# Kernel tuning notes

Hardware: AMD Instinct MI355X
Metric: run time of the kernel (lower is better)

The kernel has to match this reference:

```python
import jax, jax.numpy as jnp
import numpy as np

E = 2048      # embed_dim
HQ = 32       # num_query_heads
HKV = 8       # num_kv_heads
DH = E // HQ  # head_dim = 64
G = HQ // HKV # group_size = 4
KV_DIM = E * HKV // HQ  # 512
B, S = 2, 2048


def setup_inputs() -> dict:
    key = jax.random.key(0)
    ks = jax.random.split(key, 11)
    sc_in = 1.0 / np.sqrt(E)
    sc_attn = 1.0 / np.sqrt(E)
    return {
        "query": jax.random.normal(ks[0], (B, S, E), jnp.float32),
        "key": jax.random.normal(ks[1], (B, S, E), jnp.float32),
        "value": jax.random.normal(ks[2], (B, S, E), jnp.float32),
        "Wq": jax.random.normal(ks[3], (E, E), jnp.float32) * sc_in,
        "bq": jnp.zeros((E,), jnp.float32),
        "Wk": jax.random.normal(ks[4], (E, KV_DIM), jnp.float32) * sc_in,
        "bk": jnp.zeros((KV_DIM,), jnp.float32),
        "Wv": jax.random.normal(ks[5], (E, KV_DIM), jnp.float32) * sc_in,
        "bv": jnp.zeros((KV_DIM,), jnp.float32),
        "Wo": jax.random.normal(ks[6], (E, E), jnp.float32) * sc_attn,
        "bo": jnp.zeros((E,), jnp.float32),
    }


def reference(query, key, value, Wq, bq, Wk, bk, Wv, bv, Wo, bo):
    b, s, _ = query.shape
    # projections
    Q = (query @ Wq + bq).reshape(b, s, HQ, DH).transpose(0, 2, 1, 3)   # [B,HQ,S,DH]
    K = (key @ Wk + bk).reshape(b, s, HKV, DH).transpose(0, 2, 1, 3)    # [B,HKV,S,DH]
    V = (value @ Wv + bv).reshape(b, s, HKV, DH).transpose(0, 2, 1, 3)  # [B,HKV,S,DH]
    # GQA: repeat_interleave along head dim (kv head h -> query heads h*G..h*G+G-1)
    K = jnp.repeat(K, G, axis=1)  # [B,HQ,S,DH]
    V = jnp.repeat(V, G, axis=1)  # [B,HQ,S,DH]
    scores = jnp.einsum('bhqd,bhkd->bhqk', Q, K) / np.sqrt(DH).astype(np.float32)
    attn_weights = jax.nn.softmax(scores, axis=-1)                      # [B,HQ,S,S]
    attn_out = jnp.einsum('bhqk,bhkd->bhqd', attn_weights, V)           # [B,HQ,S,DH]
    attn_out = attn_out.transpose(0, 2, 1, 3).reshape(b, s, E)
    out = attn_out @ Wo + bo
    return out, attn_weights
```

## Files before the change

kernel.cpp:

```cpp
#include <hip/hip_runtime.h>
#include <stdint.h>

typedef _Float16 f16;
typedef _Float16 f16x8 __attribute__((ext_vector_type(8)));
typedef _Float16 f16x4 __attribute__((ext_vector_type(4)));
typedef float    f32x4 __attribute__((ext_vector_type(4)));

#define SEQ   2048
#define EDIM  2048
#define NHQ   32
#define NHKV  8
#define DHEAD 64
#define KVD   512
#define NB    2
#define NTOK  (NB*SEQ)
#define SCALE 0.1803368801111204f

__device__ __forceinline__ f32x4 mfma16(f16x8 a, f16x8 b, f32x4 c) {
  return __builtin_amdgcn_mfma_f32_16x16x32_f16(a, b, c, 0, 0, 0);
}

__device__ __forceinline__ void gload_lds16(const void* g, void* l) {
  __builtin_amdgcn_global_load_lds(
      (const __attribute__((address_space(1))) void*)g,
      (__attribute__((address_space(3))) void*)l, 16, 0, 0);
}

__global__ __launch_bounds__(256) void k_cvt3(const float* __restrict__ s0,
                                              const float* __restrict__ s1,
                                              const float* __restrict__ s2,
                                              f16* __restrict__ d) {
  int i = blockIdx.x * 256 + threadIdx.x;
  int t = i >> 21, j = i & ((1 << 21) - 1);
  const float* s = (t == 0) ? s0 : ((t == 1) ? s1 : s2);
  float4 v = reinterpret_cast<const float4*>(s)[j];
  f16x4 h;
  h[0] = (f16)v.x; h[1] = (f16)v.y; h[2] = (f16)v.z; h[3] = (f16)v.w;
  reinterpret_cast<f16x4*>(d)[i] = h;
}

__global__ __launch_bounds__(256) void k_tconv(const float* __restrict__ s0,
                                               const float* __restrict__ s1,
                                               f16* __restrict__ d0,
                                               f16* __restrict__ d1,
                                               int R, int C) {
  const float* s = blockIdx.z ? s1 : s0;
  f16* d = blockIdx.z ? d1 : d0;
  __shared__ float t[32][33];
  int tr = blockIdx.x, tc = blockIdx.y;
  int lr = threadIdx.x >> 3;
  int lc = (threadIdx.x & 7) << 2;
  float4 v = *reinterpret_cast<const float4*>(&s[(size_t)(tr*32+lr)*C + tc*32 + lc]);
  t[lr][lc+0] = v.x; t[lr][lc+1] = v.y; t[lr][lc+2] = v.z; t[lr][lc+3] = v.w;
  __syncthreads();
  f16x4 h;
  h[0] = (f16)t[lc+0][lr];
  h[1] = (f16)t[lc+1][lr];
  h[2] = (f16)t[lc+2][lr];
  h[3] = (f16)t[lc+3][lr];
  *reinterpret_cast<f16x4*>(&d[(size_t)(tc*32+lr)*R + tr*32 + lc]) = h;
}

__global__ __launch_bounds__(256) void k_trv(const f16* __restrict__ src,
                                             f16* __restrict__ dst) {
  __shared__ f16 t[64][68];
  int bh = blockIdx.x;
  int st = blockIdx.y;
  int b = bh >> 3, h = bh & 7;
  #pragma unroll
  for (int i = 0; i < 4; ++i) {
    int sl = i*16 + (threadIdx.x >> 4);
    int d4 = (threadIdx.x & 15) * 4;
    *(f16x4*)&t[sl][d4] =
        *(const f16x4*)&src[(size_t)(b*SEQ + st*64 + sl)*KVD + h*DHEAD + d4];
  }
  __syncthreads();
  #pragma unroll
  for (int i = 0; i < 4; ++i) {
    int dl = i*16 + (threadIdx.x >> 4);
    int s4 = (threadIdx.x & 15) * 4;
    f16x4 v;
    v[0] = t[s4+0][dl]; v[1] = t[s4+1][dl]; v[2] = t[s4+2][dl]; v[3] = t[s4+3][dl];
    *(f16x4*)&dst[(size_t)(bh*DHEAD + dl)*SEQ + st*64 + s4] = v;
  }
}

template<int F16OUT>
__global__ __launch_bounds__(256) void k_gemm(
    const f16* __restrict__ A0, const f16* __restrict__ A1,
    const f16* __restrict__ Bt0, const f16* __restrict__ Bt1,
    const float* __restrict__ bias0, const float* __restrict__ bias1,
    void* __restrict__ C0, void* __restrict__ C1,
    int M, int N, int K)
{
  const f16* A    = blockIdx.z ? A1 : A0;
  const f16* Bt   = blockIdx.z ? Bt1 : Bt0;
  const float* bias = blockIdx.z ? bias1 : bias0;
  void* Cout      = blockIdx.z ? C1 : C0;

  __shared__ f16 sA[128*64];
  __shared__ f16 sB[128*64];
  const int tid  = threadIdx.x;
  const int lane = tid & 63, wv = tid >> 6;
  const int tn = blockIdx.x, tm = blockIdx.y;
  const int wm = wv >> 1, wn = wv & 1;
  const int l15 = lane & 15, lhi = lane >> 4;

  const f32x4 zz = {0.f, 0.f, 0.f, 0.f};
  f32x4 acc[4][4];
  #pragma unroll
  for (int m = 0; m < 4; ++m)
    #pragma unroll
    for (int n = 0; n < 4; ++n) acc[m][n] = zz;

  const f16* gsrc[8];
  f16* ldst[8];
  #pragma unroll
  for (int i = 0; i < 8; ++i) {
    int u = wv*8 + i;
    int r  = (u & 15)*8 + (lane >> 3);
    int cb = ((lane & 7) << 4) ^ ((r & 7) << 4);
    if (u < 16) {
      gsrc[i] = A  + (size_t)(tm*128 + r)*K + (cb >> 1);
      ldst[i] = sA + u*512;
    } else {
      gsrc[i] = Bt + (size_t)(tn*128 + r)*K + (cb >> 1);
      ldst[i] = sB + (u - 16)*512;
    }
  }

  int aoff[2][4], boff[2][4];
  #pragma unroll
  for (int ks = 0; ks < 2; ++ks)
    #pragma unroll
    for (int m = 0; m < 4; ++m) {
      int ra = wm*64 + m*16 + l15;
      aoff[ks][m] = ra*128 + ((ks*64 + (lhi << 4)) ^ ((ra & 7) << 4));
      int rb = wn*64 + m*16 + l15;
      boff[ks][m] = rb*128 + ((ks*64 + (lhi << 4)) ^ ((rb & 7) << 4));
    }

  const int nkb = K >> 6;
  for (int kb = 0; kb < nkb; ++kb) {
    #pragma unroll
    for (int i = 0; i < 8; ++i)
      gload_lds16(gsrc[i] + kb*64, ldst[i]);
    __syncthreads();
    #pragma unroll
    for (int ks = 0; ks < 2; ++ks) {
      f16x8 af[4], bf[4];
      #pragma unroll
      for (int m = 0; m < 4; ++m)
        af[m] = *(const f16x8*)((const char*)sA + aoff[ks][m]);
      #pragma unroll
      for (int n = 0; n < 4; ++n)
        bf[n] = *(const f16x8*)((const char*)sB + boff[ks][n]);
      #pragma unroll
      for (int m = 0; m < 4; ++m)
        #pragma unroll
        for (int n = 0; n < 4; ++n)
          acc[m][n] = mfma16(af[m], bf[n], acc[m][n]);
    }
    __syncthreads();
  }

  float bcol[4];
  #pragma unroll
  for (int n = 0; n < 4; ++n)
    bcol[n] = bias[tn*128 + wn*64 + n*16 + l15];
  #pragma unroll
  for (int m = 0; m < 4; ++m)
    #pragma unroll
    for (int n = 0; n < 4; ++n)
      #pragma unroll
      for (int r = 0; r < 4; ++r) {
        int row = tm*128 + wm*64 + m*16 + lhi*4 + r;
        int col = tn*128 + wn*64 + n*16 + l15;
        float v = acc[m][n][r] + bcol[n];
        if (F16OUT) ((f16*)Cout)[(size_t)row*N + col] = (f16)v;
        else        ((float*)Cout)[(size_t)row*N + col] = v;
      }
}

__global__ __launch_bounds__(256) void k_attn(
    const f16* __restrict__ Qp,
    const f16* __restrict__ Kp,
    const f16* __restrict__ Vt,
    float* __restrict__ wout,
    f16* __restrict__ AO)
{
  __shared__ f16 sK[2][64*64];
  __shared__ f16 sV[2][64*64];
  __shared__ f16 sW[4][16*64];
  const int tid = threadIdx.x, lane = tid & 63, wv = tid >> 6;
  const int bid = (blockIdx.x & 7) * 256 + (blockIdx.x >> 3);
  const int b = bid >> 10, h = (bid >> 5) & 31, qb = bid & 31;
  const int hk = h >> 2;
  const int l15 = lane & 15, lhi = lane >> 4;
  const int rloc = (lane >> 3) & 7, chk = lane & 7;
  const int csw = (chk ^ rloc) * 8;
  const int sw  = (l15 & 7) << 4;
  const int qrow0 = qb*64 + wv*16;
  const f32x4 zz = {0.f, 0.f, 0.f, 0.f};

  f16x8 qf[2];
  #pragma unroll
  for (int ks = 0; ks < 2; ++ks)
    qf[ks] = *(const f16x8*)&Qp[(size_t)(b*SEQ + qrow0 + l15)*EDIM
                                + h*DHEAD + ks*32 + lhi*8];

  const f16* Kb = Kp + (size_t)(b*SEQ)*KVD + hk*DHEAD;
  const f16* Vb = Vt + (size_t)((b*NHKV + hk)*DHEAD)*SEQ;

  float lsum = 0.f;
  {
    #pragma unroll
    for (int i = 0; i < 2; ++i) {
      int u = wv*2 + i;
      gload_lds16(Kb + (size_t)(u*8 + rloc)*KVD + csw, &sK[0][u*512]);
    }
    __syncthreads();
    int buf = 0;
    for (int kb = 0; kb < SEQ/64; ++kb) {
      if (kb < SEQ/64 - 1) {
        #pragma unroll
        for (int i = 0; i < 2; ++i) {
          int u = wv*2 + i;
          gload_lds16(Kb + (size_t)((kb+1)*64 + u*8 + rloc)*KVD + csw, &sK[buf^1][u*512]);
        }
      }
      #pragma unroll
      for (int kt = 0; kt < 4; ++kt) {
        const char* kbase = (const char*)&sK[buf][0] + (kt*16 + l15)*128;
        f16x8 kf0 = *(const f16x8*)(kbase + ((lhi*16) ^ sw));
        f16x8 kf1 = *(const f16x8*)(kbase + ((64 + lhi*16) ^ sw));
        f32x4 s = zz;
        s = mfma16(kf0, qf[0], s);
        s = mfma16(kf1, qf[1], s);
        #pragma unroll
        for (int r = 0; r < 4; ++r)
          lsum += __builtin_amdgcn_exp2f(s[r] * SCALE);
      }
      __syncthreads();
      buf ^= 1;
    }
  }
  float den = lsum;
  den += __shfl_xor(den, 16);
  den += __shfl_xor(den, 32);
  const float rinv = __builtin_amdgcn_rcpf(den);

  f32x4 o[4];
  #pragma unroll
  for (int dt = 0; dt < 4; ++dt) o[dt] = zz;

  f16* swv = &sW[wv][0];
  float* wrow = wout + (size_t)((b*NHQ + h)*SEQ + qrow0)*SEQ;

  {
    #pragma unroll
    for (int i = 0; i < 2; ++i) {
      int u = wv*2 + i;
      gload_lds16(Kb + (size_t)(u*8 + rloc)*KVD + csw, &sK[0][u*512]);
      gload_lds16(Vb + (size_t)(u*8 + rloc)*SEQ + csw, &sV[0][u*512]);
    }
    __syncthreads();
    int buf = 0;
    for (int kb = 0; kb < SEQ/64; ++kb) {
      if (kb < SEQ/64 - 1) {
        #pragma unroll
        for (int i = 0; i < 2; ++i) {
          int u = wv*2 + i;
          gload_lds16(Kb + (size_t)((kb+1)*64 + u*8 + rloc)*KVD + csw, &sK[buf^1][u*512]);
          gload_lds16(Vb + (size_t)(u*8 + rloc)*SEQ + (kb+1)*64 + csw, &sV[buf^1][u*512]);
        }
      }
      #pragma unroll
      for (int kt = 0; kt < 4; ++kt) {
        const char* kbase = (const char*)&sK[buf][0] + (kt*16 + l15)*128;
        f16x8 kf0 = *(const f16x8*)(kbase + ((lhi*16) ^ sw));
        f16x8 kf1 = *(const f16x8*)(kbase + ((64 + lhi*16) ^ sw));
        f32x4 s = zz;
        s = mfma16(kf0, qf[0], s);
        s = mfma16(kf1, qf[1], s);
        f32x4 wvec;
        f16x4 wh;
        #pragma unroll
        for (int r = 0; r < 4; ++r) {
          float w = __builtin_amdgcn_exp2f(s[r] * SCALE) * rinv;
          wvec[r] = w;
          wh[r] = (f16)w;
        }
        __builtin_nontemporal_store(wvec,
            (f32x4*)(wrow + (size_t)l15*SEQ + kb*64 + kt*16 + lhi*4));
        *(f16x4*)((char*)swv + l15*128 + ((kt*32 + lhi*8) ^ sw)) = wh;
      }
      #pragma unroll
      for (int ks = 0; ks < 2; ++ks) {
        f16x8 af = *(const f16x8*)((const char*)swv + l15*128 + ((ks*64 + lhi*16) ^ sw));
        #pragma unroll
        for (int dt = 0; dt < 4; ++dt) {
          const char* vbase = (const char*)&sV[buf][0] + (dt*16 + l15)*128;
          f16x8 vf = *(const f16x8*)(vbase + ((ks*64 + lhi*16) ^ sw));
          o[dt] = mfma16(af, vf, o[dt]);
        }
      }
      __syncthreads();
      buf ^= 1;
    }
  }

  #pragma unroll
  for (int dt = 0; dt < 4; ++dt)
    #pragma unroll
    for (int r = 0; r < 4; ++r)
      AO[(size_t)(b*SEQ + qrow0 + lhi*4 + r)*EDIM + h*DHEAD + dt*16 + l15]
          = (f16)o[dt][r];
}

extern "C" void kernel_launch(void* const* d_in, const int* in_sizes, int n_in,
                              void* d_out, int out_size, void* d_ws, size_t ws_size,
                              hipStream_t stream) {
  (void)in_sizes; (void)n_in; (void)out_size; (void)ws_size;
  const float* query = (const float*)d_in[0];
  const float* key   = (const float*)d_in[1];
  const float* value = (const float*)d_in[2];
  const float* Wq    = (const float*)d_in[3];
  const float* bq    = (const float*)d_in[4];
  const float* Wk    = (const float*)d_in[5];
  const float* bk    = (const float*)d_in[6];
  const float* Wv    = (const float*)d_in[7];
  const float* bv    = (const float*)d_in[8];
  const float* Wo    = (const float*)d_in[9];
  const float* bo    = (const float*)d_in[10];

  float* out   = (float*)d_out;
  float* wattn = out + (size_t)NTOK*EDIM;

  f16* p   = (f16*)d_ws;
  f16* q16 = p;  p += (size_t)NTOK*EDIM;
  f16* k16 = p;  p += (size_t)NTOK*EDIM;
  f16* v16 = p;  p += (size_t)NTOK*EDIM;
  f16* wqT = p;  p += (size_t)EDIM*EDIM;
  f16* wkT = p;  p += (size_t)KVD*EDIM;
  f16* wvT = p;  p += (size_t)KVD*EDIM;
  f16* woT = p;  p += (size_t)EDIM*EDIM;
  f16* Qp  = p;  p += (size_t)NTOK*EDIM;
  f16* Kp  = p;  p += (size_t)NTOK*KVD;
  f16* Vp  = p;  p += (size_t)NTOK*KVD;
  f16* Vt  = p;  p += (size_t)NTOK*KVD;
  f16* AO  = p;  p += (size_t)NTOK*EDIM;

  k_cvt3<<<3*(NTOK*EDIM/4)/256, 256, 0, stream>>>(query, key, value, q16);

  k_tconv<<<dim3(EDIM/32, EDIM/32, 2), 256, 0, stream>>>(Wq, Wo, wqT, woT, EDIM, EDIM);
  k_tconv<<<dim3(EDIM/32, KVD/32, 2),  256, 0, stream>>>(Wk, Wv, wkT, wvT, EDIM, KVD);

  k_gemm<1><<<dim3(EDIM/128, NTOK/128, 1), 256, 0, stream>>>(
      q16, q16, wqT, wqT, bq, bq, Qp, Qp, NTOK, EDIM, EDIM);
  k_gemm<1><<<dim3(KVD/128, NTOK/128, 2), 256, 0, stream>>>(
      k16, v16, wkT, wvT, bk, bv, Kp, Vp, NTOK, KVD, EDIM);

  k_trv<<<dim3(NB*NHKV, SEQ/64), 256, 0, stream>>>(Vp, Vt);

  k_attn<<<NB*NHQ*(SEQ/64), 256, 0, stream>>>(Qp, Kp, Vt, wattn, AO);

  k_gemm<0><<<dim3(EDIM/128, NTOK/128, 1), 256, 0, stream>>>(
      AO, AO, woT, woT, bo, bo, out, out, NTOK, EDIM, EDIM);
}
```

Baseline: 508.5 us.

## Fuse QKV projections into one 256-tile pipelined GEMM and deepen attention prefetch

Replaces the 128x128 GEMM with a 256-row, 512-thread GEMM that runs a 4-stage LDS pipeline with explicit vmcnt waits. Q, K and V projections now run as a single launch writing one packed QKV buffer, relying on wqT/wkT/wvT being contiguous so they form a 3072-column B matrix. The attention kernel reads from the packed layout and replaces its trailing __syncthreads with a partial vmcnt wait plus barrier so prefetches can stay in flight. The aim is more operand reuse per tile, fewer launches and more load/compute overlap. The cost is higher register and LDS pressure, and the manual waitcnt counts and the workspace layout both have to be exactly right.

```diff
diff --git a/kernel.cpp b/kernel.cpp
--- a/kernel.cpp
+++ b/kernel.cpp
@@ -14,6 +14,7 @@
 #define KVD   512
 #define NB    2
 #define NTOK  (NB*SEQ)
+#define QKVN  3072
 #define SCALE 0.1803368801111204f
 
 __device__ __forceinline__ f32x4 mfma16(f16x8 a, f16x8 b, f32x4 c) {
@@ -61,7 +62,7 @@
   *reinterpret_cast<f16x4*>(&d[(size_t)(tc*32+lr)*R + tr*32 + lc]) = h;
 }
 
-__global__ __launch_bounds__(256) void k_trv(const f16* __restrict__ src,
+__global__ __launch_bounds__(256) void k_trv(const f16* __restrict__ qkv,
                                              f16* __restrict__ dst) {
   __shared__ f16 t[64][68];
   int bh = blockIdx.x;
@@ -72,7 +73,7 @@
     int sl = i*16 + (threadIdx.x >> 4);
     int d4 = (threadIdx.x & 15) * 4;
     *(f16x4*)&t[sl][d4] =
-        *(const f16x4*)&src[(size_t)(b*SEQ + st*64 + sl)*KVD + h*DHEAD + d4];
+        *(const f16x4*)&qkv[(size_t)(b*SEQ + st*64 + sl)*QKVN + 2560 + h*DHEAD + d4];
   }
   __syncthreads();
   #pragma unroll
@@ -85,106 +86,132 @@
   }
 }
 
-template<int F16OUT>
-__global__ __launch_bounds__(256) void k_gemm(
-    const f16* __restrict__ A0, const f16* __restrict__ A1,
-    const f16* __restrict__ Bt0, const f16* __restrict__ Bt1,
-    const float* __restrict__ bias0, const float* __restrict__ bias1,
-    void* __restrict__ C0, void* __restrict__ C1,
-    int M, int N, int K)
+template<int BN, int F16OUT, int NTN>
+__global__ __launch_bounds__(512, 2) void k_gemm256(
+    const f16* __restrict__ Abase, const f16* __restrict__ Bt,
+    const float* __restrict__ bq, const float* __restrict__ bk,
+    const float* __restrict__ bv, void* __restrict__ Cout)
 {
-  const f16* A    = blockIdx.z ? A1 : A0;
-  const f16* Bt   = blockIdx.z ? Bt1 : Bt0;
-  const float* bias = blockIdx.z ? bias1 : bias0;
-  void* Cout      = blockIdx.z ? C1 : C0;
-
-  __shared__ f16 sA[128*64];
-  __shared__ f16 sB[128*64];
-  const int tid  = threadIdx.x;
-  const int lane = tid & 63, wv = tid >> 6;
-  const int tn = blockIdx.x, tm = blockIdx.y;
-  const int wm = wv >> 1, wn = wv & 1;
+  constexpr int K   = EDIM;
+  constexpr int NT  = K / 32;
+  constexpr int NLB = BN / 128;
+  constexpr int NI  = BN / 64;
+  constexpr int NCOL = NTN * BN;
+
+  __shared__ f16 sA[4][256*32];
+  __shared__ f16 sB[4][BN*32];
+
+  const int tid = threadIdx.x, lane = tid & 63, w = tid >> 6;
+  const int cpx = gridDim.x >> 3;
+  const int flat = blockIdx.x;
+  const int tid2 = (flat & 7) * cpx + (flat >> 3);
+  const int tn = tid2 % NTN, tm = tid2 / NTN;
+
+  int sel = 0, coff = 0;
+  if (BN == 256) { sel = (tn >= 8) + (tn >= 10); coff = sel == 0 ? 0 : (sel == 1 ? 2048 : 2560); }
+  const f16* A = Abase + (size_t)sel * NTOK * EDIM;
+  const float* bias = sel == 0 ? bq : (sel == 1 ? bk : bv);
+
+  const int wm = w >> 2, wn = w & 3;
   const int l15 = lane & 15, lhi = lane >> 4;
 
+  const f16* gA[2]; int uA[2];
+  #pragma unroll
+  for (int r = 0; r < 2; ++r) {
+    int row = r*128 + w*16 + (lane >> 2);
+    gA[r] = A + (size_t)(tm*256 + row)*K + (((lane & 3) ^ (row & 3)) << 3);
+    uA[r] = row * 32;
+  }
+  const f16* gB[NLB]; int uB[NLB];
+  #pragma unroll
+  for (int r = 0; r < NLB; ++r) {
+    int row = r*128 + w*16 + (lane >> 2);
+    gB[r] = Bt + (size_t)(tn*BN + row)*K + (((lane & 3) ^ (row & 3)) << 3);
+    uB[r] = row * 32;
+  }
+
+  int aoff[8], boff[NI];
+  #pragma unroll
+  for (int mi = 0; mi < 8; ++mi)
+    aoff[mi] = (wm*128 + mi*16 + l15)*64 + ((lhi ^ (l15 & 3)) << 4);
+  #pragma unroll
+  for (int ni = 0; ni < NI; ++ni)
+    boff[ni] = (wn*(BN/4) + ni*16 + l15)*64 + ((lhi ^ (l15 & 3)) << 4);
+
   const f32x4 zz = {0.f, 0.f, 0.f, 0.f};
-  f32x4 acc[4][4];
-  #pragma unroll
-  for (int m = 0; m < 4; ++m)
-    #pragma unroll
-    for (int n = 0; n < 4; ++n) acc[m][n] = zz;
-
-  const f16* gsrc[8];
-  f16* ldst[8];
-  #pragma unroll
-  for (int i = 0; i < 8; ++i) {
-    int u = wv*8 + i;
-    int r  = (u & 15)*8 + (lane >> 3);
-    int cb = ((lane & 7) << 4) ^ ((r & 7) << 4);
-    if (u < 16) {
-      gsrc[i] = A  + (size_t)(tm*128 + r)*K + (cb >> 1);
-      ldst[i] = sA + u*512;
-    } else {
-      gsrc[i] = Bt + (size_t)(tn*128 + r)*K + (cb >> 1);
-      ldst[i] = sB + (u - 16)*512;
-    }
-  }
-
-  int aoff[2][4], boff[2][4];
-  #pragma unroll
-  for (int ks = 0; ks < 2; ++ks)
-    #pragma unroll
-    for (int m = 0; m < 4; ++m) {
-      int ra = wm*64 + m*16 + l15;
-      aoff[ks][m] = ra*128 + ((ks*64 + (lhi << 4)) ^ ((ra & 7) << 4));
-      int rb = wn*64 + m*16 + l15;
-      boff[ks][m] = rb*128 + ((ks*64 + (lhi << 4)) ^ ((rb & 7) << 4));
-    }
-
-  const int nkb = K >> 6;
-  for (int kb = 0; kb < nkb; ++kb) {
-    #pragma unroll
-    for (int i = 0; i < 8; ++i)
-      gload_lds16(gsrc[i] + kb*64, ldst[i]);
-    __syncthreads();
-    #pragma unroll
-    for (int ks = 0; ks < 2; ++ks) {
-      f16x8 af[4], bf[4];
-      #pragma unroll
-      for (int m = 0; m < 4; ++m)
-        af[m] = *(const f16x8*)((const char*)sA + aoff[ks][m]);
-      #pragma unroll
-      for (int n = 0; n < 4; ++n)
-        bf[n] = *(const f16x8*)((const char*)sB + boff[ks][n]);
-      #pragma unroll
-      for (int m = 0; m < 4; ++m)
-        #pragma unroll
-        for (int n = 0; n < 4; ++n)
-          acc[m][n] = mfma16(af[m], bf[n], acc[m][n]);
-    }
-    __syncthreads();
-  }
-
-  float bcol[4];
-  #pragma unroll
-  for (int n = 0; n < 4; ++n)
-    bcol[n] = bias[tn*128 + wn*64 + n*16 + l15];
-  #pragma unroll
-  for (int m = 0; m < 4; ++m)
-    #pragma unroll
-    for (int n = 0; n < 4; ++n)
+  f32x4 acc[8][NI];
+  #pragma unroll
+  for (int mi = 0; mi < 8; ++mi)
+    #pragma unroll
+    for (int ni = 0; ni < NI; ++ni) acc[mi][ni] = zz;
+
+  auto STAGE = [&](int t) {
+    int sl = t & 3;
+    #pragma unroll
+    for (int r = 0; r < 2; ++r)   gload_lds16(gA[r] + t*32, &sA[sl][uA[r]]);
+    #pragma unroll
+    for (int r = 0; r < NLB; ++r) gload_lds16(gB[r] + t*32, &sB[sl][uB[r]]);
+  };
+  auto COMP = [&](int t) {
+    int sl = t & 3;
+    const char* ba = (const char*)&sA[sl][0];
+    const char* bb = (const char*)&sB[sl][0];
+    f16x8 af[8], bf[NI];
+    #pragma unroll
+    for (int ni = 0; ni < NI; ++ni) bf[ni] = *(const f16x8*)(bb + boff[ni]);
+    #pragma unroll
+    for (int mi = 0; mi < 8; ++mi)  af[mi] = *(const f16x8*)(ba + aoff[mi]);
+    #pragma unroll
+    for (int mi = 0; mi < 8; ++mi)
+      #pragma unroll
+      for (int ni = 0; ni < NI; ++ni)
+        acc[mi][ni] = mfma16(af[mi], bf[ni], acc[mi][ni]);
+  };
+
+  STAGE(0); STAGE(1); STAGE(2);
+  for (int t = 0; t < NT - 3; ++t) {
+    if (BN == 256) asm volatile("s_waitcnt vmcnt(8)" ::: "memory");
+    else           asm volatile("s_waitcnt vmcnt(6)" ::: "memory");
+    __builtin_amdgcn_s_barrier();
+    __builtin_amdgcn_sched_barrier(0);
+    STAGE(t + 3);
+    COMP(t);
+  }
+  if (BN == 256) asm volatile("s_waitcnt vmcnt(8)" ::: "memory");
+  else           asm volatile("s_waitcnt vmcnt(6)" ::: "memory");
+  __builtin_amdgcn_s_barrier();
+  __builtin_amdgcn_sched_barrier(0);
+  COMP(NT - 3);
+  if (BN == 256) asm volatile("s_waitcnt vmcnt(4)" ::: "memory");
+  else           asm volatile("s_waitcnt vmcnt(3)" ::: "memory");
+  __builtin_amdgcn_s_barrier();
+  __builtin_amdgcn_sched_barrier(0);
+  COMP(NT - 2);
+  asm volatile("s_waitcnt vmcnt(0)" ::: "memory");
+  __builtin_amdgcn_s_barrier();
+  __builtin_amdgcn_sched_barrier(0);
+  COMP(NT - 1);
+
+  float bcol[NI];
+  #pragma unroll
+  for (int ni = 0; ni < NI; ++ni)
+    bcol[ni] = bias[tn*BN + wn*(BN/4) + ni*16 + l15 - coff];
+  #pragma unroll
+  for (int mi = 0; mi < 8; ++mi)
+    #pragma unroll
+    for (int ni = 0; ni < NI; ++ni)
       #pragma unroll
       for (int r = 0; r < 4; ++r) {
-        int row = tm*128 + wm*64 + m*16 + lhi*4 + r;
-        int col = tn*128 + wn*64 + n*16 + l15;
-        float v = acc[m][n][r] + bcol[n];
-        if (F16OUT) ((f16*)Cout)[(size_t)row*N + col] = (f16)v;
-        else        ((float*)Cout)[(size_t)row*N + col] = v;
+        int row = tm*256 + wm*128 + mi*16 + lhi*4 + r;
+        int col = tn*BN + wn*(BN/4) + ni*16 + l15;
+        float v = acc[mi][ni][r] + bcol[ni];
+        if (F16OUT) ((f16*)Cout)[(size_t)row*NCOL + col] = (f16)v;
+        else        ((float*)Cout)[(size_t)row*NCOL + col] = v;
       }
 }
 
 __global__ __launch_bounds__(256) void k_attn(
-    const f16* __restrict__ Qp,
-    const f16* __restrict__ Kp,
+    const f16* __restrict__ QKV,
     const f16* __restrict__ Vt,
     float* __restrict__ wout,
     f16* __restrict__ AO)
@@ -206,10 +233,10 @@
   f16x8 qf[2];
   #pragma unroll
   for (int ks = 0; ks < 2; ++ks)
-    qf[ks] = *(const f16x8*)&Qp[(size_t)(b*SEQ + qrow0 + l15)*EDIM
-                                + h*DHEAD + ks*32 + lhi*8];
-
-  const f16* Kb = Kp + (size_t)(b*SEQ)*KVD + hk*DHEAD;
+    qf[ks] = *(const f16x8*)&QKV[(size_t)(b*SEQ + qrow0 + l15)*QKVN
+                                 + h*DHEAD + ks*32 + lhi*8];
+
+  const f16* Kb = QKV + 2048 + (size_t)(b*SEQ)*QKVN + hk*DHEAD;
   const f16* Vb = Vt + (size_t)((b*NHKV + hk)*DHEAD)*SEQ;
 
   float lsum = 0.f;
@@ -217,7 +244,7 @@
     #pragma unroll
     for (int i = 0; i < 2; ++i) {
       int u = wv*2 + i;
-      gload_lds16(Kb + (size_t)(u*8 + rloc)*KVD + csw, &sK[0][u*512]);
+      gload_lds16(Kb + (size_t)(u*8 + rloc)*QKVN + csw, &sK[0][u*512]);
     }
     __syncthreads();
     int buf = 0;
@@ -226,7 +253,7 @@
         #pragma unroll
         for (int i = 0; i < 2; ++i) {
           int u = wv*2 + i;
-          gload_lds16(Kb + (size_t)((kb+1)*64 + u*8 + rloc)*KVD + csw, &sK[buf^1][u*512]);
+          gload_lds16(Kb + (size_t)((kb+1)*64 + u*8 + rloc)*QKVN + csw, &sK[buf^1][u*512]);
         }
       }
       #pragma unroll
@@ -261,7 +288,7 @@
     #pragma unroll
     for (int i = 0; i < 2; ++i) {
       int u = wv*2 + i;
-      gload_lds16(Kb + (size_t)(u*8 + rloc)*KVD + csw, &sK[0][u*512]);
+      gload_lds16(Kb + (size_t)(u*8 + rloc)*QKVN + csw, &sK[0][u*512]);
       gload_lds16(Vb + (size_t)(u*8 + rloc)*SEQ + csw, &sV[0][u*512]);
     }
     __syncthreads();
@@ -271,10 +298,11 @@
         #pragma unroll
         for (int i = 0; i < 2; ++i) {
           int u = wv*2 + i;
-          gload_lds16(Kb + (size_t)((kb+1)*64 + u*8 + rloc)*KVD + csw, &sK[buf^1][u*512]);
+          gload_lds16(Kb + (size_t)((kb+1)*64 + u*8 + rloc)*QKVN + csw, &sK[buf^1][u*512]);
           gload_lds16(Vb + (size_t)(u*8 + rloc)*SEQ + (kb+1)*64 + csw, &sV[buf^1][u*512]);
         }
       }
+      __builtin_amdgcn_sched_barrier(0);
       #pragma unroll
       for (int kt = 0; kt < 4; ++kt) {
         const char* kbase = (const char*)&sK[buf][0] + (kt*16 + l15)*128;
@@ -287,9 +315,9 @@
         f16x4 wh;
         #pragma unroll
         for (int r = 0; r < 4; ++r) {
-          float w = __builtin_amdgcn_exp2f(s[r] * SCALE) * rinv;
-          wvec[r] = w;
-          wh[r] = (f16)w;
+          float wgt = __builtin_amdgcn_exp2f(s[r] * SCALE) * rinv;
+          wvec[r] = wgt;
+          wh[r] = (f16)wgt;
         }
         __builtin_nontemporal_store(wvec,
             (f32x4*)(wrow + (size_t)l15*SEQ + kb*64 + kt*16 + lhi*4));
@@ -305,7 +333,9 @@
           o[dt] = mfma16(af, vf, o[dt]);
         }
       }
-      __syncthreads();
+      asm volatile("s_waitcnt vmcnt(4)" ::: "memory");
+      __builtin_amdgcn_s_barrier();
+      __builtin_amdgcn_sched_barrier(0);
       buf ^= 1;
     }
   }
@@ -337,34 +367,28 @@
   float* out   = (float*)d_out;
   float* wattn = out + (size_t)NTOK*EDIM;
 
-  f16* p   = (f16*)d_ws;
-  f16* q16 = p;  p += (size_t)NTOK*EDIM;
-  f16* k16 = p;  p += (size_t)NTOK*EDIM;
-  f16* v16 = p;  p += (size_t)NTOK*EDIM;
-  f16* wqT = p;  p += (size_t)EDIM*EDIM;
-  f16* wkT = p;  p += (size_t)KVD*EDIM;
-  f16* wvT = p;  p += (size_t)KVD*EDIM;
-  f16* woT = p;  p += (size_t)EDIM*EDIM;
-  f16* Qp  = p;  p += (size_t)NTOK*EDIM;
-  f16* Kp  = p;  p += (size_t)NTOK*KVD;
-  f16* Vp  = p;  p += (size_t)NTOK*KVD;
-  f16* Vt  = p;  p += (size_t)NTOK*KVD;
-  f16* AO  = p;  p += (size_t)NTOK*EDIM;
+  f16* p    = (f16*)d_ws;
+  f16* q16  = p;  p += (size_t)NTOK*EDIM;
+  f16* k16  = p;  p += (size_t)NTOK*EDIM;
+  f16* v16  = p;  p += (size_t)NTOK*EDIM;
+  f16* wqT  = p;  p += (size_t)EDIM*EDIM;
+  f16* wkT  = p;  p += (size_t)KVD*EDIM;
+  f16* wvT  = p;  p += (size_t)KVD*EDIM;
+  f16* woT  = p;  p += (size_t)EDIM*EDIM;
+  f16* QKVp = p;  p += (size_t)NTOK*QKVN;
+  f16* Vt   = p;  p += (size_t)NTOK*KVD;
+  f16* AO   = p;  p += (size_t)NTOK*EDIM;
 
   k_cvt3<<<3*(NTOK*EDIM/4)/256, 256, 0, stream>>>(query, key, value, q16);
 
   k_tconv<<<dim3(EDIM/32, EDIM/32, 2), 256, 0, stream>>>(Wq, Wo, wqT, woT, EDIM, EDIM);
   k_tconv<<<dim3(EDIM/32, KVD/32, 2),  256, 0, stream>>>(Wk, Wv, wkT, wvT, EDIM, KVD);
 
-  k_gemm<1><<<dim3(EDIM/128, NTOK/128, 1), 256, 0, stream>>>(
-      q16, q16, wqT, wqT, bq, bq, Qp, Qp, NTOK, EDIM, EDIM);
-  k_gemm<1><<<dim3(KVD/128, NTOK/128, 2), 256, 0, stream>>>(
-      k16, v16, wkT, wvT, bk, bv, Kp, Vp, NTOK, KVD, EDIM);
-
-  k_trv<<<dim3(NB*NHKV, SEQ/64), 256, 0, stream>>>(Vp, Vt);
-
-  k_attn<<<NB*NHQ*(SEQ/64), 256, 0, stream>>>(Qp, Kp, Vt, wattn, AO);
-
-  k_gemm<0><<<dim3(EDIM/128, NTOK/128, 1), 256, 0, stream>>>(
-      AO, AO, woT, woT, bo, bo, out, out, NTOK, EDIM, EDIM);
-}
+  k_gemm256<256, 1, 12><<<192, 512, 0, stream>>>(q16, wqT, bq, bk, bv, QKVp);
+
+  k_trv<<<dim3(NB*NHKV, SEQ/64), 256, 0, stream>>>(QKVp, Vt);
+
+  k_attn<<<NB*NHQ*(SEQ/64), 256, 0, stream>>>(QKVp, Vt, wattn, AO);
+
+  k_gemm256<128, 0, 16><<<256, 512, 0, stream>>>(AO, woT, bo, bo, bo, out);
+}
```

Result: slower. 541.3 us (+6.5%).
